# Kernel tuning notes

Measured on AMD Instinct MI355X. Metric: run time of the kernel, lower is better.

The kernel has to match this reference:

```python
import jax, jax.numpy as jnp
import numpy as np

DN = ('NCHW', 'OIHW', 'NCHW')

def conv2d(x, w, b, stride=1, pad=1):
    y = jax.lax.conv_general_dilated(x, w, (stride, stride), ((pad, pad), (pad, pad)),
                                     dimension_numbers=DN)
    return y + b[None, :, None, None]

def deconv2d(x, w, b):
    # PyTorch ConvTranspose2d(k=3, s=2, p=1, output_padding=1): weight is (I, O, kh, kw);
    # equivalent to conv with lhs_dilation=2, pad (k-1-p, k-1-p+output_padding)=(1,2), flipped kernel.
    wt = jnp.flip(w, (2, 3)).transpose(1, 0, 2, 3)  # -> (O, I, kh, kw)
    y = jax.lax.conv_general_dilated(x, wt, (1, 1), ((1, 2), (1, 2)),
                                     lhs_dilation=(2, 2), dimension_numbers=DN)
    return y + b[None, :, None, None]

def gru_cell(x, h, wg, bg, wc, bc):
    # standard ConvGRU: gates from cat(x, h), candidate from cat(x, r*h)
    g = jax.nn.sigmoid(conv2d(jnp.concatenate([x, h], axis=1), wg, bg, 1, 1))
    r, u = jnp.split(g, 2, axis=1)
    c = jnp.tanh(conv2d(jnp.concatenate([x, r * h], axis=1), wc, bc, 1, 1))
    return u * h + (1.0 - u) * c

def setup_inputs() -> dict:
    key = jax.random.key(0)
    ks = jax.random.split(key, 20)
    C_IN, BC = 32, 8  # in_channels, base_channels
    B, D, H, W = 1, 48, 256, 320
    s = 0.05
    def w(k, shape):
        return jax.random.normal(k, shape, jnp.float32) * s
    return {
        'volume_variance': jax.random.normal(ks[0], (B, C_IN, D, H, W), jnp.float32),
        'conv1_w': w(ks[1], (BC, C_IN, 3, 3)),       'conv1_b': jnp.zeros((BC,), jnp.float32),
        'gru1_wg': w(ks[2], (2 * BC, 2 * BC, 3, 3)), 'gru1_bg': jnp.zeros((2 * BC,), jnp.float32),
        'gru1_wc': w(ks[3], (BC, 2 * BC, 3, 3)),     'gru1_bc': jnp.zeros((BC,), jnp.float32),
        'conv2_w': w(ks[4], (2 * BC, BC, 3, 3)),     'conv2_b': jnp.zeros((2 * BC,), jnp.float32),
        'gru2_wg': w(ks[5], (4 * BC, 4 * BC, 3, 3)), 'gru2_bg': jnp.zeros((4 * BC,), jnp.float32),
        'gru2_wc': w(ks[6], (2 * BC, 4 * BC, 3, 3)), 'gru2_bc': jnp.zeros((2 * BC,), jnp.float32),
        'up1_w': w(ks[7], (2 * BC, BC, 3, 3)),       'up1_b': jnp.zeros((BC,), jnp.float32),   # ConvTranspose (I,O,kh,kw)
        'up2_w': w(ks[8], (BC, 1, 3, 3)),            'up2_b': jnp.zeros((1,), jnp.float32),
    }

def reference(volume_variance, conv1_w, conv1_b, gru1_wg, gru1_bg, gru1_wc, gru1_bc,
              conv2_w, conv2_b, gru2_wg, gru2_bg, gru2_wc, gru2_bc,
              up1_w, up1_b, up2_w, up2_b):
    B, F, D, H, W = volume_variance.shape
    dt = volume_variance.dtype
    xs = jnp.moveaxis(volume_variance, 2, 0)  # (D, B, F, H, W)
    s1 = jnp.zeros((B, 8, H, W), dt)
    s2 = jnp.zeros((B, 16, H // 2, W // 2), dt)

    def step(carry, cost):
        s1, s2 = carry
        c1 = jax.nn.relu(conv2d(cost, conv1_w, conv1_b, 1, 1))
        s1 = gru_cell(c1, s1, gru1_wg, gru1_bg, gru1_wc, gru1_bc)
        c2 = jax.nn.relu(conv2d(s1, conv2_w, conv2_b, 2, 1))
        s2 = gru_cell(c2, s2, gru2_wg, gru2_bg, gru2_wc, gru2_bc)
        up1 = deconv2d(s2, up1_w, up1_b)          # back to (B, 8, H, W)
        u = jax.nn.relu(up1 + s1)
        out = deconv2d(u, up2_w, up2_b)           # (B, 1, 2H, 2W)
        return (s1, s2), out

    _, outs = jax.lax.scan(step, (s1, s2), xs)    # outs: (D, B, 1, 2H, 2W)
    return jnp.moveaxis(outs[:, :, 0], 0, 1)      # (B, D, 2H, 2W)
```

## Files before the change

kernel.cpp:

```cpp
#include <hip/hip_runtime.h>

#define DD 48
#define HF 256
#define WF 320
#define HH 128
#define WH 160
#define NPF (HF * WF)
#define NPH (HH * WH)
#define S1SZ (8 * NPF)
#define S2SZ (16 * NPH)

__device__ __forceinline__ float sigf(float x) { return 1.0f / (1.0f + __expf(-x)); }
__device__ __forceinline__ float tanh_(float x) {
    float e = __expf(2.0f * x);
    return 1.0f - 2.0f / (e + 1.0f);
}


template<int Ht, int Wt>
__device__ __forceinline__ void taps2(int y, int x0, int* off, float* msk) {
    int cx[4]; float cm[4];
    cx[0] = max(x0 - 1, 0);      cm[0] = (x0 > 0) ? 1.0f : 0.0f;
    cx[1] = x0;                  cm[1] = 1.0f;
    cx[2] = x0 + 1;              cm[2] = 1.0f;
    cx[3] = min(x0 + 2, Wt - 1); cm[3] = (x0 + 2 < Wt) ? 1.0f : 0.0f;
#pragma unroll
    for (int r = 0; r < 3; ++r) {
        int yy = y - 1 + r;
        float rm = ((unsigned)yy < (unsigned)Ht) ? 1.0f : 0.0f;
        int rb = min(max(yy, 0), Ht - 1) * Wt;
#pragma unroll
        for (int k = 0; k < 4; ++k) {
            off[r * 4 + k] = rb + cx[k];
            msk[r * 4 + k] = rm * cm[k];
        }
    }
}

template<int CI, int COUT>
__device__ __forceinline__ void acc2px(
    const float* __restrict__ in, int cs,
    const float* __restrict__ w, int wcs,
    const int* off, const float* msk,
    float* a0, float* a1)
{
#pragma unroll 2
    for (int ci = 0; ci < CI; ++ci) {
        const float* p = in + ci * cs;
        float v[12];
#pragma unroll
        for (int k = 0; k < 12; ++k) v[k] = p[off[k]] * msk[k];
        const float* wp = w + ci * 9;
#pragma unroll
        for (int j = 0; j < COUT; ++j) {
            const float* wc = wp + j * wcs;
#pragma unroll
            for (int r = 0; r < 3; ++r) {
                a0[j] = fmaf(v[r * 4 + 0], wc[r * 3 + 0], a0[j]);
                a0[j] = fmaf(v[r * 4 + 1], wc[r * 3 + 1], a0[j]);
                a0[j] = fmaf(v[r * 4 + 2], wc[r * 3 + 2], a0[j]);
                a1[j] = fmaf(v[r * 4 + 1], wc[r * 3 + 0], a1[j]);
                a1[j] = fmaf(v[r * 4 + 2], wc[r * 3 + 1], a1[j]);
                a1[j] = fmaf(v[r * 4 + 3], wc[r * 3 + 2], a1[j]);
            }
        }
    }
}

__global__ __launch_bounds__(256) void k_conv1(
    const float* __restrict__ x, const float* __restrict__ w,
    const float* __restrict__ b, float* __restrict__ out,
    int d0, int ostride)
{
    const int t = blockIdx.x * 256 + threadIdx.x;
    const int xc = t % WF;
    const int yb = (t / WF) * 4;
    const float* __restrict__ xin = x + (long)(d0 + blockIdx.z) * NPF;
    const int cxm = max(xc - 1, 0), cxp = min(xc + 1, WF - 1);
    const float cmm = (xc > 0) ? 1.0f : 0.0f;
    const float cmp = (xc < WF - 1) ? 1.0f : 0.0f;
    int off[18]; float msk[18];
#pragma unroll
    for (int r = 0; r < 6; ++r) {
        const int yy = yb - 1 + r;
        const float rm = ((unsigned)yy < (unsigned)HF) ? 1.0f : 0.0f;
        const int rb = min(max(yy, 0), HF - 1) * WF;
        off[r * 3 + 0] = rb + cxm; msk[r * 3 + 0] = rm * cmm;
        off[r * 3 + 1] = rb + xc;  msk[r * 3 + 1] = rm;
        off[r * 3 + 2] = rb + cxp; msk[r * 3 + 2] = rm * cmp;
    }
    float acc[4][8];
#pragma unroll
    for (int j = 0; j < 8; ++j) {
        const float bj = b[j];
#pragma unroll
        for (int q = 0; q < 4; ++q) acc[q][j] = bj;
    }
#pragma unroll 2
    for (int ci = 0; ci < 32; ++ci) {
        const float* p = xin + (long)ci * (DD * NPF);
        float v[18];
#pragma unroll
        for (int k = 0; k < 18; ++k) v[k] = p[off[k]] * msk[k];
        const float* wp = w + ci * 9;
#pragma unroll
        for (int j = 0; j < 8; ++j) {
            const float* wc = wp + j * (32 * 9);
#pragma unroll
            for (int q = 0; q < 4; ++q) {
#pragma unroll
                for (int r = 0; r < 3; ++r) {
                    acc[q][j] = fmaf(v[(q + r) * 3 + 0], wc[r * 3 + 0], acc[q][j]);
                    acc[q][j] = fmaf(v[(q + r) * 3 + 1], wc[r * 3 + 1], acc[q][j]);
                    acc[q][j] = fmaf(v[(q + r) * 3 + 2], wc[r * 3 + 2], acc[q][j]);
                }
            }
        }
    }
    float* o = out + (long)blockIdx.z * ostride + yb * WF + xc;
#pragma unroll
    for (int j = 0; j < 8; ++j)
#pragma unroll
        for (int q = 0; q < 4; ++q)
            o[j * NPF + q * WF] = fmaxf(acc[q][j], 0.0f);
}

template<int C, int Ht, int Wt, int CO>
__device__ __forceinline__ void gates_role(
    const float* __restrict__ a, const float* __restrict__ s,
    const float* __restrict__ w, const float* __restrict__ b,
    float* __restrict__ rh, float* __restrict__ u, int pb, int cog)
{
    constexpr int NP = Ht * Wt;
    const int pix0 = (pb * 256 + threadIdx.x) * 2;
    const int y = pix0 / Wt, x0 = pix0 - y * Wt;
    const int co0 = cog * CO;
    int off[12]; float msk[12];
    taps2<Ht, Wt>(y, x0, off, msk);
    float a0[CO], a1[CO];
#pragma unroll
    for (int j = 0; j < CO; ++j) { a0[j] = b[co0 + j]; a1[j] = b[co0 + j]; }
    acc2px<C, CO>(a, NP, w + co0 * (2 * C * 9), 2 * C * 9, off, msk, a0, a1);
    acc2px<C, CO>(s, NP, w + co0 * (2 * C * 9) + C * 9, 2 * C * 9, off, msk, a0, a1);
    if (co0 < C) {
#pragma unroll
        for (int j = 0; j < CO; ++j) {
            int o = (co0 + j) * NP + pix0;
            rh[o]     = sigf(a0[j]) * s[o];
            rh[o + 1] = sigf(a1[j]) * s[o + 1];
        }
    } else {
#pragma unroll
        for (int j = 0; j < CO; ++j) {
            int o = (co0 - C + j) * NP + pix0;
            u[o]     = sigf(a0[j]);
            u[o + 1] = sigf(a1[j]);
        }
    }
}

template<int C, int Ht, int Wt, int CO>
__device__ __forceinline__ void cand_role(
    const float* __restrict__ a, const float* __restrict__ rh,
    const float* __restrict__ w, const float* __restrict__ b,
    const float* __restrict__ u, const float* __restrict__ sprev,
    float* __restrict__ sout, int pb, int cog)
{
    constexpr int NP = Ht * Wt;
    const int pix0 = (pb * 256 + threadIdx.x) * 2;
    const int y = pix0 / Wt, x0 = pix0 - y * Wt;
    const int co0 = cog * CO;
    int off[12]; float msk[12];
    taps2<Ht, Wt>(y, x0, off, msk);
    float a0[CO], a1[CO];
#pragma unroll
    for (int j = 0; j < CO; ++j) { a0[j] = b[co0 + j]; a1[j] = b[co0 + j]; }
    acc2px<C, CO>(a, NP, w + co0 * (2 * C * 9), 2 * C * 9, off, msk, a0, a1);
    acc2px<C, CO>(rh, NP, w + co0 * (2 * C * 9) + C * 9, 2 * C * 9, off, msk, a0, a1);
#pragma unroll
    for (int j = 0; j < CO; ++j) {
        int o = (co0 + j) * NP + pix0;
        float c0 = tanh_(a0[j]);
        float c1 = tanh_(a1[j]);
        sout[o]     = fmaf(u[o],     sprev[o]     - c0, c0);
        sout[o + 1] = fmaf(u[o + 1], sprev[o + 1] - c1, c1);
    }
}

__device__ __forceinline__ void conv2_role(
    const float* __restrict__ s1, const float* __restrict__ w,
    const float* __restrict__ b, float* __restrict__ c2, int pb, int cog)
{
    const int pix0 = (pb * 256 + threadIdx.x) * 2;
    const int y = pix0 / WH, x0 = pix0 - y * WH;
    const int co0 = cog * 8;
    int off[15]; float msk[15];
    {
        int cx[5]; float cm[5];
        cx[0] = max(2 * x0 - 1, 0); cm[0] = (x0 > 0) ? 1.0f : 0.0f;
#pragma unroll
        for (int i = 1; i < 5; ++i) { cx[i] = 2 * x0 - 1 + i; cm[i] = 1.0f; }
#pragma unroll
        for (int r = 0; r < 3; ++r) {
            int yy = 2 * y - 1 + r;
            float rm = ((unsigned)yy < (unsigned)HF) ? 1.0f : 0.0f;
            int rb = min(max(yy, 0), HF - 1) * WF;
#pragma unroll
            for (int i = 0; i < 5; ++i) { off[r * 5 + i] = rb + cx[i]; msk[r * 5 + i] = rm * cm[i]; }
        }
    }
    float a0[8], a1[8];
#pragma unroll
    for (int j = 0; j < 8; ++j) { a0[j] = b[co0 + j]; a1[j] = b[co0 + j]; }
#pragma unroll 2
    for (int ci = 0; ci < 8; ++ci) {
        const float* p = s1 + ci * NPF;
        float v[15];
#pragma unroll
        for (int k = 0; k < 15; ++k) v[k] = p[off[k]] * msk[k];
        const float* wp = w + co0 * 72 + ci * 9;
#pragma unroll
        for (int j = 0; j < 8; ++j) {
            const float* wc = wp + j * 72;
#pragma unroll
            for (int r = 0; r < 3; ++r) {
                a0[j] = fmaf(v[r * 5 + 0], wc[r * 3 + 0], a0[j]);
                a0[j] = fmaf(v[r * 5 + 1], wc[r * 3 + 1], a0[j]);
                a0[j] = fmaf(v[r * 5 + 2], wc[r * 3 + 2], a0[j]);
                a1[j] = fmaf(v[r * 5 + 2], wc[r * 3 + 0], a1[j]);
                a1[j] = fmaf(v[r * 5 + 3], wc[r * 3 + 1], a1[j]);
                a1[j] = fmaf(v[r * 5 + 4], wc[r * 3 + 2], a1[j]);
            }
        }
    }
#pragma unroll
    for (int j = 0; j < 8; ++j) {
        c2[(co0 + j) * NPH + pix0]     = fmaxf(a0[j], 0.0f);
        c2[(co0 + j) * NPH + pix0 + 1] = fmaxf(a1[j], 0.0f);
    }
}

__global__ __launch_bounds__(256) void k_stepA(
    const float* __restrict__ c1_all, const float* __restrict__ s1_all,
    const float* __restrict__ wg1, const float* __restrict__ bg1,
    float* __restrict__ rh1, float* __restrict__ ug1,
    const float* __restrict__ c2_all, const float* __restrict__ s2_all,
    const float* __restrict__ wg2, const float* __restrict__ bg2,
    float* __restrict__ rh2, float* __restrict__ ug2,
    int d1, int d2)
{
    const int bid = blockIdx.x;
    if (bid < 320) {
        if (d1 < 0) return;
        gates_role<8, HF, WF, 8>(c1_all + (long)d1 * S1SZ, s1_all + (long)d1 * S1SZ,
                                 wg1, bg1, rh1, ug1, bid % 160, bid / 160);
    } else {
        if (d2 < 0) return;
        const int bb = bid - 320;
        gates_role<16, HH, WH, 4>(c2_all + (long)d2 * S2SZ, s2_all + (long)d2 * S2SZ,
                                  wg2, bg2, rh2, ug2, bb % 40, bb / 40);
    }
}

__global__ __launch_bounds__(256) void k_stepB(
    const float* __restrict__ c1_all, float* __restrict__ s1_all,
    const float* __restrict__ wc1, const float* __restrict__ bc1,
    const float* __restrict__ rh1, const float* __restrict__ ug1,
    const float* __restrict__ w2, const float* __restrict__ b2,
    float* __restrict__ c2_all, float* __restrict__ s2_all,
    const float* __restrict__ wc2, const float* __restrict__ bc2,
    const float* __restrict__ rh2, const float* __restrict__ ug2,
    int d1, int dc, int d2)
{
    const int bid = blockIdx.x;
    if (bid < 160) {
        if (d1 < 0) return;
        cand_role<8, HF, WF, 8>(c1_all + (long)d1 * S1SZ, rh1, wc1, bc1, ug1,
                                s1_all + (long)d1 * S1SZ, s1_all + (long)(d1 + 1) * S1SZ,
                                bid, 0);
    } else if (bid < 240) {
        if (dc < 0) return;
        const int bb = bid - 160;
        conv2_role(s1_all + (long)(dc + 1) * S1SZ, w2, b2,
                   c2_all + (long)dc * S2SZ, bb % 40, bb / 40);
    } else {
        if (d2 < 0) return;
        const int bb = bid - 240;
        cand_role<16, HH, WH, 4>(c2_all + (long)d2 * S2SZ, rh2, wc2, bc2, ug2,
                                 s2_all + (long)d2 * S2SZ, s2_all + (long)(d2 + 1) * S2SZ,
                                 bb % 40, bb / 40);
    }
}

template<int C, int Ht, int Wt, int CO>
__global__ __launch_bounds__(256) void k_gates(
    const float* __restrict__ a, const float* __restrict__ s,
    const float* __restrict__ w, const float* __restrict__ b,
    float* __restrict__ rh, float* __restrict__ u)
{ gates_role<C, Ht, Wt, CO>(a, s, w, b, rh, u, blockIdx.x, blockIdx.y); }

template<int C, int Ht, int Wt, int CO>
__global__ __launch_bounds__(256) void k_cand(
    const float* __restrict__ a, const float* __restrict__ rh,
    const float* __restrict__ w, const float* __restrict__ b,
    const float* __restrict__ u, const float* __restrict__ sprev,
    float* __restrict__ sout)
{ cand_role<C, Ht, Wt, CO>(a, rh, w, b, u, sprev, sout, blockIdx.x, blockIdx.y); }

__global__ __launch_bounds__(256) void k_conv2w(
    const float* __restrict__ s1, const float* __restrict__ w,
    const float* __restrict__ b, float* __restrict__ c2)
{ conv2_role(s1, w, b, c2, blockIdx.x, blockIdx.y); }

__global__ __launch_bounds__(256) void k_up1(
    const float* __restrict__ s2b, int zs2,
    const float* __restrict__ w, const float* __restrict__ b,
    const float* __restrict__ s1b, int zs1,
    float* __restrict__ ub, int zu)
{
    const int q = blockIdx.x * 256 + threadIdx.x;
    const int r = q / WH, c = q - r * WH;
    const float* s2 = s2b + blockIdx.z * zs2;
    const float* s1 = s1b + blockIdx.z * zs1;
    float* ubuf = ub + blockIdx.z * zu;
    const int dc = (c + 1 < WH) ? 1 : 0;
    const int dr = (r + 1 < HH) ? WH : 0;
    const float mc = (c + 1 < WH) ? 1.0f : 0.0f;
    const float mr = (r + 1 < HH) ? 1.0f : 0.0f;
    const float mrc = mc * mr;
    float a00[8], a01[8], a10[8], a11[8];
#pragma unroll
    for (int j = 0; j < 8; ++j) { a00[j] = b[j]; a01[j] = b[j]; a10[j] = b[j]; a11[j] = b[j]; }
#pragma unroll 2
    for (int ci = 0; ci < 16; ++ci) {
        const float* p = s2 + ci * NPH + r * WH + c;
        float v00 = p[0];
        float v01 = p[dc] * mc;
        float v10 = p[dr] * mr;
        float v11 = p[dr + dc] * mrc;
        const float* wp = w + ci * 8 * 9;
#pragma unroll
        for (int j = 0; j < 8; ++j) {
            const float* wc = wp + j * 9;
            a00[j] = fmaf(v00, wc[4], a00[j]);
            a01[j] = fmaf(v01, wc[3], fmaf(v00, wc[5], a01[j]));
            a10[j] = fmaf(v10, wc[1], fmaf(v00, wc[7], a10[j]));
            a11[j] = fmaf(v11, wc[0], fmaf(v10, wc[2], fmaf(v01, wc[6], fmaf(v00, wc[8], a11[j]))));
        }
    }
    const int o0 = (2 * r) * WF + 2 * c;
#pragma unroll
    for (int j = 0; j < 8; ++j) {
        int o = j * NPF + o0;
        ubuf[o]          = fmaxf(a00[j] + s1[o], 0.0f);
        ubuf[o + 1]      = fmaxf(a01[j] + s1[o + 1], 0.0f);
        ubuf[o + WF]     = fmaxf(a10[j] + s1[o + WF], 0.0f);
        ubuf[o + WF + 1] = fmaxf(a11[j] + s1[o + WF + 1], 0.0f);
    }
}

__global__ __launch_bounds__(256) void k_up2(
    const float* __restrict__ ub, int zu,
    const float* __restrict__ w, const float* __restrict__ b,
    float* __restrict__ out, int d0)
{
    const int q = blockIdx.x * 256 + threadIdx.x;
    const int r = q / WF, c = q - r * WF;
    const float* u = ub + blockIdx.z * zu;
    const int dc = (c + 1 < WF) ? 1 : 0;
    const int dr = (r + 1 < HF) ? WF : 0;
    const float mc = (c + 1 < WF) ? 1.0f : 0.0f;
    const float mr = (r + 1 < HF) ? 1.0f : 0.0f;
    const float mrc = mc * mr;
    const float b0 = b[0];
    float a00 = b0, a01 = b0, a10 = b0, a11 = b0;
#pragma unroll 2
    for (int ci = 0; ci < 8; ++ci) {
        const float* p = u + ci * NPF + r * WF + c;
        float v00 = p[0];
        float v01 = p[dc] * mc;
        float v10 = p[dr] * mr;
        float v11 = p[dr + dc] * mrc;
        const float* wc = w + ci * 9;
        a00 = fmaf(v00, wc[4], a00);
        a01 = fmaf(v01, wc[3], fmaf(v00, wc[5], a01));
        a10 = fmaf(v10, wc[1], fmaf(v00, wc[7], a10));
        a11 = fmaf(v11, wc[0], fmaf(v10, wc[2], fmaf(v01, wc[6], fmaf(v00, wc[8], a11))));
    }
    float* o = out + (long)(d0 + blockIdx.z) * (512 * 640) + (2 * r) * 640 + 2 * c;
    o[0] = a00; o[1] = a01; o[640] = a10; o[641] = a11;
}

extern "C" void kernel_launch(void* const* d_in, const int* in_sizes, int n_in,
                              void* d_out, int out_size, void* d_ws, size_t ws_size,
                              hipStream_t stream)
{
    const float* x   = (const float*)d_in[0];
    const float* w1  = (const float*)d_in[1];
    const float* b1  = (const float*)d_in[2];
    const float* wg1 = (const float*)d_in[3];
    const float* bg1 = (const float*)d_in[4];
    const float* wc1 = (const float*)d_in[5];
    const float* bc1 = (const float*)d_in[6];
    const float* w2  = (const float*)d_in[7];
    const float* b2  = (const float*)d_in[8];
    const float* wg2 = (const float*)d_in[9];
    const float* bg2 = (const float*)d_in[10];
    const float* wc2 = (const float*)d_in[11];
    const float* bc2 = (const float*)d_in[12];
    const float* wu1 = (const float*)d_in[13];
    const float* bu1 = (const float*)d_in[14];
    const float* wu2 = (const float*)d_in[15];
    const float* bu2 = (const float*)d_in[16];
    float* out = (float*)d_out;
    float* ws = (float*)d_ws;

    {
        float* p = ws;
        float* s1_all = p; p += 49L * S1SZ;
        float* s2_all = p; p += 49L * S2SZ;
        float* c2_all = p; p += 48L * S2SZ;
        float* rh1 = p; p += S1SZ;
        float* ug1 = p; p += S1SZ;
        float* rh2 = p; p += S2SZ;
        float* ug2 = p; p += S2SZ;
        float* c1_all = p; p += 48L * S1SZ;
        const size_t need = (size_t)(p - ws) * sizeof(float);
        if (ws_size >= need) {
            float* u_all = c1_all;
            hipMemsetAsync(s1_all, 0, (size_t)S1SZ * sizeof(float), stream);
            hipMemsetAsync(s2_all, 0, (size_t)S2SZ * sizeof(float), stream);

            k_conv1<<<dim3(80, 1, 48), 256, 0, stream>>>(x, w1, b1, c1_all, 0, S1SZ);
            for (int d = 0; d < 50; ++d) {
                const int g1 = (d < 48) ? d : -1;
                const int g2 = (d >= 2) ? d - 2 : -1;
                const int cv = (d >= 1 && d <= 48) ? d - 1 : -1;
                k_stepA<<<dim3(640), 256, 0, stream>>>(
                    c1_all, s1_all, wg1, bg1, rh1, ug1,
                    c2_all, s2_all, wg2, bg2, rh2, ug2, g1, g2);
                k_stepB<<<dim3(400), 256, 0, stream>>>(
                    c1_all, s1_all, wc1, bc1, rh1, ug1,
                    w2, b2, c2_all, s2_all, wc2, bc2, rh2, ug2,
                    g1, cv, g2);
            }
            k_up1<<<dim3(80, 1, 48), 256, 0, stream>>>(s2_all + S2SZ, S2SZ, wu1, bu1,
                                                       s1_all + S1SZ, S1SZ, u_all, S1SZ);
            k_up2<<<dim3(320, 1, 48), 256, 0, stream>>>(u_all, S1SZ, wu2, bu2, out, 0);
            return;
        }
    }

    {
        float* p = ws;
        float* s1 = p; p += S1SZ;
        float* s2 = p; p += S2SZ;
        float* rh1 = p; p += S1SZ;
        float* ug1 = p; p += S1SZ;
        float* c2 = p; p += S2SZ;
        float* rh2 = p; p += S2SZ;
        float* ug2 = p; p += S2SZ;
        float* c1 = p; p += S1SZ;
        float* u = p; p += S1SZ;
        hipMemsetAsync(s1, 0, (size_t)S1SZ * sizeof(float), stream);
        hipMemsetAsync(s2, 0, (size_t)S2SZ * sizeof(float), stream);
        for (int d = 0; d < 48; ++d) {
            k_conv1<<<dim3(80, 1, 1), 256, 0, stream>>>(x, w1, b1, c1, d, 0);
            k_gates<8, HF, WF, 8><<<dim3(160, 2), 256, 0, stream>>>(c1, s1, wg1, bg1, rh1, ug1);
            k_cand <8, HF, WF, 8><<<dim3(160, 1), 256, 0, stream>>>(c1, rh1, wc1, bc1, ug1, s1, s1);
            k_conv2w<<<dim3(40, 2), 256, 0, stream>>>(s1, w2, b2, c2);
            k_gates<16, HH, WH, 8><<<dim3(40, 4), 256, 0, stream>>>(c2, s2, wg2, bg2, rh2, ug2);
            k_cand <16, HH, WH, 8><<<dim3(40, 2), 256, 0, stream>>>(c2, rh2, wc2, bc2, ug2, s2, s2);
            k_up1<<<dim3(80, 1, 1), 256, 0, stream>>>(s2, 0, wu1, bu1, s1, 0, u, 0);
            k_up2<<<dim3(320, 1, 1), 256, 0, stream>>>(u, 0, wu2, bu2, out, d);
        }
    }
}
```

Measured before the change: 3.630 ms.

## Fold conv1, up1 and up2 into the per-step wavefront kernels

The up-front batched conv1 and the trailing batched up1/up2 passes are replaced by extra block roles inside the per-depth stepA/stepB kernels. Each role works on a skewed depth index, so conv1 runs two slices ahead and the upsampling runs a few slices behind, all inside the same launches. This fills idle CUs in the small recurrent steps and avoids streaming large all-depth intermediate buffers, with u now held in a single-slice buffer. The cost is one extra wavefront step, bigger grids and more role branching.

```diff
diff --git a/kernel.cpp b/kernel.cpp
--- a/kernel.cpp
+++ b/kernel.cpp
@@ -16,7 +16,6 @@
     return 1.0f - 2.0f / (e + 1.0f);
 }
 
-
 template<int Ht, int Wt>
 __device__ __forceinline__ void taps2(int y, int x0, int* off, float* msk) {
     int cx[4]; float cm[4];
@@ -67,15 +66,15 @@
     }
 }
 
-__global__ __launch_bounds__(256) void k_conv1(
+__device__ __forceinline__ void conv1_role(
     const float* __restrict__ x, const float* __restrict__ w,
-    const float* __restrict__ b, float* __restrict__ out,
-    int d0, int ostride)
-{
-    const int t = blockIdx.x * 256 + threadIdx.x;
+    const float* __restrict__ b, float* __restrict__ o_slice,
+    int dsl, int pb)
+{
+    const int t = pb * 256 + threadIdx.x;
     const int xc = t % WF;
     const int yb = (t / WF) * 4;
-    const float* __restrict__ xin = x + (long)(d0 + blockIdx.z) * NPF;
+    const float* __restrict__ xin = x + (long)dsl * NPF;
     const int cxm = max(xc - 1, 0), cxp = min(xc + 1, WF - 1);
     const float cmm = (xc > 0) ? 1.0f : 0.0f;
     const float cmp = (xc < WF - 1) ? 1.0f : 0.0f;
@@ -117,12 +116,20 @@
             }
         }
     }
-    float* o = out + (long)blockIdx.z * ostride + yb * WF + xc;
+    float* o = o_slice + yb * WF + xc;
 #pragma unroll
     for (int j = 0; j < 8; ++j)
 #pragma unroll
         for (int q = 0; q < 4; ++q)
             o[j * NPF + q * WF] = fmaxf(acc[q][j], 0.0f);
+}
+
+__global__ __launch_bounds__(256) void k_conv1(
+    const float* __restrict__ x, const float* __restrict__ w,
+    const float* __restrict__ b, float* __restrict__ out,
+    int d0, int ostride)
+{
+    conv1_role(x, w, b, out + (long)blockIdx.z * ostride, d0 + blockIdx.z, blockIdx.x);
 }
 
 template<int C, int Ht, int Wt, int CO>
@@ -240,89 +247,13 @@
     }
 }
 
-__global__ __launch_bounds__(256) void k_stepA(
-    const float* __restrict__ c1_all, const float* __restrict__ s1_all,
-    const float* __restrict__ wg1, const float* __restrict__ bg1,
-    float* __restrict__ rh1, float* __restrict__ ug1,
-    const float* __restrict__ c2_all, const float* __restrict__ s2_all,
-    const float* __restrict__ wg2, const float* __restrict__ bg2,
-    float* __restrict__ rh2, float* __restrict__ ug2,
-    int d1, int d2)
-{
-    const int bid = blockIdx.x;
-    if (bid < 320) {
-        if (d1 < 0) return;
-        gates_role<8, HF, WF, 8>(c1_all + (long)d1 * S1SZ, s1_all + (long)d1 * S1SZ,
-                                 wg1, bg1, rh1, ug1, bid % 160, bid / 160);
-    } else {
-        if (d2 < 0) return;
-        const int bb = bid - 320;
-        gates_role<16, HH, WH, 4>(c2_all + (long)d2 * S2SZ, s2_all + (long)d2 * S2SZ,
-                                  wg2, bg2, rh2, ug2, bb % 40, bb / 40);
-    }
-}
-
-__global__ __launch_bounds__(256) void k_stepB(
-    const float* __restrict__ c1_all, float* __restrict__ s1_all,
-    const float* __restrict__ wc1, const float* __restrict__ bc1,
-    const float* __restrict__ rh1, const float* __restrict__ ug1,
-    const float* __restrict__ w2, const float* __restrict__ b2,
-    float* __restrict__ c2_all, float* __restrict__ s2_all,
-    const float* __restrict__ wc2, const float* __restrict__ bc2,
-    const float* __restrict__ rh2, const float* __restrict__ ug2,
-    int d1, int dc, int d2)
-{
-    const int bid = blockIdx.x;
-    if (bid < 160) {
-        if (d1 < 0) return;
-        cand_role<8, HF, WF, 8>(c1_all + (long)d1 * S1SZ, rh1, wc1, bc1, ug1,
-                                s1_all + (long)d1 * S1SZ, s1_all + (long)(d1 + 1) * S1SZ,
-                                bid, 0);
-    } else if (bid < 240) {
-        if (dc < 0) return;
-        const int bb = bid - 160;
-        conv2_role(s1_all + (long)(dc + 1) * S1SZ, w2, b2,
-                   c2_all + (long)dc * S2SZ, bb % 40, bb / 40);
-    } else {
-        if (d2 < 0) return;
-        const int bb = bid - 240;
-        cand_role<16, HH, WH, 4>(c2_all + (long)d2 * S2SZ, rh2, wc2, bc2, ug2,
-                                 s2_all + (long)d2 * S2SZ, s2_all + (long)(d2 + 1) * S2SZ,
-                                 bb % 40, bb / 40);
-    }
-}
-
-template<int C, int Ht, int Wt, int CO>
-__global__ __launch_bounds__(256) void k_gates(
-    const float* __restrict__ a, const float* __restrict__ s,
-    const float* __restrict__ w, const float* __restrict__ b,
-    float* __restrict__ rh, float* __restrict__ u)
-{ gates_role<C, Ht, Wt, CO>(a, s, w, b, rh, u, blockIdx.x, blockIdx.y); }
-
-template<int C, int Ht, int Wt, int CO>
-__global__ __launch_bounds__(256) void k_cand(
-    const float* __restrict__ a, const float* __restrict__ rh,
-    const float* __restrict__ w, const float* __restrict__ b,
-    const float* __restrict__ u, const float* __restrict__ sprev,
-    float* __restrict__ sout)
-{ cand_role<C, Ht, Wt, CO>(a, rh, w, b, u, sprev, sout, blockIdx.x, blockIdx.y); }
-
-__global__ __launch_bounds__(256) void k_conv2w(
-    const float* __restrict__ s1, const float* __restrict__ w,
-    const float* __restrict__ b, float* __restrict__ c2)
-{ conv2_role(s1, w, b, c2, blockIdx.x, blockIdx.y); }
-
-__global__ __launch_bounds__(256) void k_up1(
-    const float* __restrict__ s2b, int zs2,
-    const float* __restrict__ w, const float* __restrict__ b,
-    const float* __restrict__ s1b, int zs1,
-    float* __restrict__ ub, int zu)
-{
-    const int q = blockIdx.x * 256 + threadIdx.x;
+__device__ __forceinline__ void up1_role(
+    const float* __restrict__ s2, const float* __restrict__ w,
+    const float* __restrict__ b, const float* __restrict__ s1,
+    float* __restrict__ ubuf, int pb)
+{
+    const int q = pb * 256 + threadIdx.x;
     const int r = q / WH, c = q - r * WH;
-    const float* s2 = s2b + blockIdx.z * zs2;
-    const float* s1 = s1b + blockIdx.z * zs1;
-    float* ubuf = ub + blockIdx.z * zu;
     const int dc = (c + 1 < WH) ? 1 : 0;
     const int dr = (r + 1 < HH) ? WH : 0;
     const float mc = (c + 1 < WH) ? 1.0f : 0.0f;
@@ -359,14 +290,12 @@
     }
 }
 
-__global__ __launch_bounds__(256) void k_up2(
-    const float* __restrict__ ub, int zu,
-    const float* __restrict__ w, const float* __restrict__ b,
-    float* __restrict__ out, int d0)
-{
-    const int q = blockIdx.x * 256 + threadIdx.x;
+__device__ __forceinline__ void up2_role(
+    const float* __restrict__ u, const float* __restrict__ w,
+    const float* __restrict__ b, float* __restrict__ oslice, int pb)
+{
+    const int q = pb * 256 + threadIdx.x;
     const int r = q / WF, c = q - r * WF;
-    const float* u = ub + blockIdx.z * zu;
     const int dc = (c + 1 < WF) ? 1 : 0;
     const int dr = (r + 1 < HF) ? WF : 0;
     const float mc = (c + 1 < WF) ? 1.0f : 0.0f;
@@ -387,8 +316,115 @@
         a10 = fmaf(v10, wc[1], fmaf(v00, wc[7], a10));
         a11 = fmaf(v11, wc[0], fmaf(v10, wc[2], fmaf(v01, wc[6], fmaf(v00, wc[8], a11))));
     }
-    float* o = out + (long)(d0 + blockIdx.z) * (512 * 640) + (2 * r) * 640 + 2 * c;
+    float* o = oslice + (2 * r) * 640 + 2 * c;
     o[0] = a00; o[1] = a01; o[640] = a10; o[641] = a11;
+}
+
+__global__ __launch_bounds__(256) void k_stepA(
+    const float* __restrict__ x, const float* __restrict__ w1,
+    const float* __restrict__ b1, float* __restrict__ c1_all,
+    const float* __restrict__ s1_all,
+    const float* __restrict__ wg1, const float* __restrict__ bg1,
+    float* __restrict__ rh1, float* __restrict__ ug1,
+    const float* __restrict__ c2_all, const float* __restrict__ s2_all,
+    const float* __restrict__ wg2, const float* __restrict__ bg2,
+    float* __restrict__ rh2, float* __restrict__ ug2,
+    const float* __restrict__ wu1, const float* __restrict__ bu1,
+    float* __restrict__ ubuf,
+    int d1, int d2, int dcv1, int du1)
+{
+    const int bid = blockIdx.x;
+    if (bid < 320) {
+        if (d1 < 0) return;
+        gates_role<8, HF, WF, 8>(c1_all + (long)d1 * S1SZ, s1_all + (long)d1 * S1SZ,
+                                 wg1, bg1, rh1, ug1, bid % 160, bid / 160);
+    } else if (bid < 640) {
+        if (d2 < 0) return;
+        const int bb = bid - 320;
+        gates_role<16, HH, WH, 4>(c2_all + (long)d2 * S2SZ, s2_all + (long)d2 * S2SZ,
+                                  wg2, bg2, rh2, ug2, bb % 40, bb / 40);
+    } else if (bid < 720) {
+        if (dcv1 < 0) return;
+        conv1_role(x, w1, b1, c1_all + (long)dcv1 * S1SZ, dcv1, bid - 640);
+    } else {
+        if (du1 < 0) return;
+        up1_role(s2_all + (long)(du1 + 1) * S2SZ, wu1, bu1,
+                 s1_all + (long)(du1 + 1) * S1SZ, ubuf, bid - 720);
+    }
+}
+
+__global__ __launch_bounds__(256) void k_stepB(
+    const float* __restrict__ c1_all, float* __restrict__ s1_all,
+    const float* __restrict__ wc1, const float* __restrict__ bc1,
+    const float* __restrict__ rh1, const float* __restrict__ ug1,
+    const float* __restrict__ w2, const float* __restrict__ b2,
+    float* __restrict__ c2_all, float* __restrict__ s2_all,
+    const float* __restrict__ wc2, const float* __restrict__ bc2,
+    const float* __restrict__ rh2, const float* __restrict__ ug2,
+    const float* __restrict__ wu2, const float* __restrict__ bu2,
+    const float* __restrict__ ubuf, float* __restrict__ out,
+    int d1, int dc, int d2, int du2)
+{
+    const int bid = blockIdx.x;
+    if (bid < 160) {
+        if (d1 < 0) return;
+        cand_role<8, HF, WF, 8>(c1_all + (long)d1 * S1SZ, rh1, wc1, bc1, ug1,
+                                s1_all + (long)d1 * S1SZ, s1_all + (long)(d1 + 1) * S1SZ,
+                                bid, 0);
+    } else if (bid < 240) {
+        if (dc < 0) return;
+        const int bb = bid - 160;
+        conv2_role(s1_all + (long)(dc + 1) * S1SZ, w2, b2,
+                   c2_all + (long)dc * S2SZ, bb % 40, bb / 40);
+    } else if (bid < 400) {
+        if (d2 < 0) return;
+        const int bb = bid - 240;
+        cand_role<16, HH, WH, 4>(c2_all + (long)d2 * S2SZ, rh2, wc2, bc2, ug2,
+                                 s2_all + (long)d2 * S2SZ, s2_all + (long)(d2 + 1) * S2SZ,
+                                 bb % 40, bb / 40);
+    } else {
+        if (du2 < 0) return;
+        up2_role(ubuf, wu2, bu2, out + (long)du2 * (512 * 640), bid - 400);
+    }
+}
+
+template<int C, int Ht, int Wt, int CO>
+__global__ __launch_bounds__(256) void k_gates(
+    const float* __restrict__ a, const float* __restrict__ s,
+    const float* __restrict__ w, const float* __restrict__ b,
+    float* __restrict__ rh, float* __restrict__ u)
+{ gates_role<C, Ht, Wt, CO>(a, s, w, b, rh, u, blockIdx.x, blockIdx.y); }
+
+template<int C, int Ht, int Wt, int CO>
+__global__ __launch_bounds__(256) void k_cand(
+    const float* __restrict__ a, const float* __restrict__ rh,
+    const float* __restrict__ w, const float* __restrict__ b,
+    const float* __restrict__ u, const float* __restrict__ sprev,
+    float* __restrict__ sout)
+{ cand_role<C, Ht, Wt, CO>(a, rh, w, b, u, sprev, sout, blockIdx.x, blockIdx.y); }
+
+__global__ __launch_bounds__(256) void k_conv2w(
+    const float* __restrict__ s1, const float* __restrict__ w,
+    const float* __restrict__ b, float* __restrict__ c2)
+{ conv2_role(s1, w, b, c2, blockIdx.x, blockIdx.y); }
+
+__global__ __launch_bounds__(256) void k_up1(
+    const float* __restrict__ s2b, int zs2,
+    const float* __restrict__ w, const float* __restrict__ b,
+    const float* __restrict__ s1b, int zs1,
+    float* __restrict__ ub, int zu)
+{
+    up1_role(s2b + (long)blockIdx.z * zs2, w, b,
+             s1b + (long)blockIdx.z * zs1, ub + (long)blockIdx.z * zu, blockIdx.x);
+}
+
+__global__ __launch_bounds__(256) void k_up2(
+    const float* __restrict__ ub, int zu,
+    const float* __restrict__ w, const float* __restrict__ b,
+    float* __restrict__ out, int d0)
+{
+    up2_role(ub + (long)blockIdx.z * zu, w, b,
+             out + (long)(d0 + blockIdx.z) * (512 * 640), blockIdx.x);
 }
 
 extern "C" void kernel_launch(void* const* d_in, const int* in_sizes, int n_in,
@@ -424,29 +460,29 @@
         float* ug1 = p; p += S1SZ;
         float* rh2 = p; p += S2SZ;
         float* ug2 = p; p += S2SZ;
+        float* ubuf = p; p += S1SZ;
         float* c1_all = p; p += 48L * S1SZ;
         const size_t need = (size_t)(p - ws) * sizeof(float);
         if (ws_size >= need) {
-            float* u_all = c1_all;
             hipMemsetAsync(s1_all, 0, (size_t)S1SZ * sizeof(float), stream);
             hipMemsetAsync(s2_all, 0, (size_t)S2SZ * sizeof(float), stream);
 
-            k_conv1<<<dim3(80, 1, 48), 256, 0, stream>>>(x, w1, b1, c1_all, 0, S1SZ);
-            for (int d = 0; d < 50; ++d) {
-                const int g1 = (d < 48) ? d : -1;
-                const int g2 = (d >= 2) ? d - 2 : -1;
-                const int cv = (d >= 1 && d <= 48) ? d - 1 : -1;
-                k_stepA<<<dim3(640), 256, 0, stream>>>(
-                    c1_all, s1_all, wg1, bg1, rh1, ug1,
-                    c2_all, s2_all, wg2, bg2, rh2, ug2, g1, g2);
-                k_stepB<<<dim3(400), 256, 0, stream>>>(
+            k_conv1<<<dim3(80, 1, 2), 256, 0, stream>>>(x, w1, b1, c1_all, 0, S1SZ);
+            for (int d = 0; d <= 50; ++d) {
+                const int g1  = (d < 48) ? d : -1;
+                const int g2  = (d >= 2 && d <= 49) ? d - 2 : -1;
+                const int cv1 = (d + 2 < 48) ? d + 2 : -1;
+                const int u1  = (d >= 3) ? d - 3 : -1;
+                const int cv  = (d >= 1 && d <= 48) ? d - 1 : -1;
+                k_stepA<<<dim3(800), 256, 0, stream>>>(
+                    x, w1, b1, c1_all, s1_all, wg1, bg1, rh1, ug1,
+                    c2_all, s2_all, wg2, bg2, rh2, ug2,
+                    wu1, bu1, ubuf, g1, g2, cv1, u1);
+                k_stepB<<<dim3(720), 256, 0, stream>>>(
                     c1_all, s1_all, wc1, bc1, rh1, ug1,
                     w2, b2, c2_all, s2_all, wc2, bc2, rh2, ug2,
-                    g1, cv, g2);
+                    wu2, bu2, ubuf, out, g1, cv, g2, u1);
             }
-            k_up1<<<dim3(80, 1, 48), 256, 0, stream>>>(s2_all + S2SZ, S2SZ, wu1, bu1,
-                                                       s1_all + S1SZ, S1SZ, u_all, S1SZ);
-            k_up2<<<dim3(320, 1, 48), 256, 0, stream>>>(u_all, S1SZ, wu2, bu2, out, 0);
             return;
         }
     }
```

Result: slower. 3.996 ms (+10.1%).
